# Performance work log

Hardware: AMD Instinct MI355X
Metric: run time of the kernel (lower is better)

The kernel has to match this reference:

```python
import jax, jax.numpy as jnp
import numpy as np

IMG = 128
NEAR, FAR = 1.0, 100.0
BG_EPS = 1e-3      # eps in soft_rasterize: background depth logit
SIGMA = 1e-6       # sigma_val
DIST_EPS = 1e-4    # dist_eps
GAMMA = 1e-6       # gamma_val
CHUNK = 500
B, V, F = 1, 5023, 10000


def setup_inputs():
    key = jax.random.key(0)
    k1, k2, k3, k4 = jax.random.split(key, 4)
    xy = jax.random.uniform(k1, (B, V, 2), minval=-1.0, maxval=1.0, dtype=jnp.float32)
    z = jax.random.uniform(k2, (B, V, 1), minval=5.0, maxval=15.0, dtype=jnp.float32)
    vertices = jnp.concatenate([xy, z], axis=-1)              # [B,V,3]
    faces = jax.random.randint(k3, (B, F, 3), 0, V, dtype=jnp.int32)
    attributes = jax.random.uniform(k4, (B, F, 3, 3), dtype=jnp.float32)
    return {"vertices": vertices, "faces": faces, "attributes": attributes}


def _seg_dist2(px, py, ax, ay, bx, by):
    # squared distance from pixel (px,py) to segment a-b; broadcasts [P] vs [B,C,1]
    dx = px - ax; dy = py - ay
    ex = bx - ax; ey = by - ay
    l2 = jnp.maximum(ex * ex + ey * ey, 1e-12)
    t = jnp.clip((dx * ex + dy * ey) / l2, 0.0, 1.0)
    rx = dx - t * ex; ry = dy - t * ey
    return rx * rx + ry * ry


def _render(vertices, faces, attributes):
    is_ = IMG
    P = is_ * is_
    bz = vertices.shape[0]
    v = vertices.at[..., 0].multiply(-1.0)                    # x flip (in-place in torch)
    fv = jax.vmap(lambda vv, ff: vv[ff])(v, faces)            # [B,F,3vert,3xyz]
    tex = attributes[..., :3]                                 # [B,F,3vert,3rgb]
    # fill_back=True: append copies with reversed winding
    fv = jnp.concatenate([fv, fv[:, :, ::-1, :]], axis=1)     # [B,2F,3,3]
    tex = jnp.concatenate([tex, tex[:, :, ::-1, :]], axis=1)
    F2 = fv.shape[1]
    pad = (-F2) % CHUNK
    valid = jnp.concatenate([jnp.ones((F2,), bool), jnp.zeros((pad,), bool)])
    fv = jnp.pad(fv, ((0, 0), (0, pad), (0, 0), (0, 0)))
    tex = jnp.pad(tex, ((0, 0), (0, pad), (0, 0), (0, 0)))
    n_chunks = (F2 + pad) // CHUNK
    fv = jnp.transpose(fv.reshape(bz, n_chunks, CHUNK, 3, 3), (1, 0, 2, 3, 4))
    tex = jnp.transpose(tex.reshape(bz, n_chunks, CHUNK, 3, 3), (1, 0, 2, 3, 4))
    valid = valid.reshape(n_chunks, CHUNK)

    # pixel centers in [-1,1]; row 0 is the top of the image (y flipped as in CUDA)
    xs = (2.0 * jnp.arange(is_, dtype=jnp.float32) + 1.0 - is_) / is_
    ys = (2.0 * (is_ - 1 - jnp.arange(is_, dtype=jnp.float32)) + 1.0 - is_) / is_
    px = jnp.broadcast_to(xs[None, :], (is_, is_)).reshape(-1)  # [P]
    py = jnp.broadcast_to(ys[:, None], (is_, is_)).reshape(-1)

    thr = DIST_EPS * SIGMA
    inv_g = 1.0 / GAMMA

    def step(carry, inp):
        m, s, cacc, prod = carry                # [B,P],[B,P],[B,3,P],[B,P]
        fvc, txc, vld = inp                     # [B,C,3,3],[B,C,3,3],[C]
        x0 = fvc[:, :, 0, 0][..., None]; y0 = fvc[:, :, 0, 1][..., None]; z0 = fvc[:, :, 0, 2][..., None]
        x1 = fvc[:, :, 1, 0][..., None]; y1 = fvc[:, :, 1, 1][..., None]; z1 = fvc[:, :, 1, 2][..., None]
        x2 = fvc[:, :, 2, 0][..., None]; y2 = fvc[:, :, 2, 1][..., None]; z2 = fvc[:, :, 2, 2][..., None]
        det = (y1 - y2) * (x0 - x2) + (x2 - x1) * (y0 - y2)   # [B,C,1]
        det = jnp.where(jnp.abs(det) < 1e-10, jnp.where(det < 0, -1e-10, 1e-10), det)
        w0 = ((y1 - y2) * (px - x2) + (x2 - x1) * (py - y2)) / det  # [B,C,P]
        w1 = ((y2 - y0) * (px - x2) + (x0 - x2) * (py - y2)) / det
        w2 = 1.0 - w0 - w1
        inside = (w0 >= 0) & (w1 >= 0) & (w2 >= 0)
        dis = jnp.minimum(jnp.minimum(_seg_dist2(px, py, x0, y0, x1, y1),
                                      _seg_dist2(px, py, x1, y1, x2, y2)),
                          _seg_dist2(px, py, x2, y2, x0, y0))     # [B,C,P] squared dist
        contrib = (inside | (dis < thr)) & vld[None, :, None]
        sgn = jnp.where(inside, 1.0, -1.0)
        Dp = jnp.where(contrib, jax.nn.sigmoid(sgn * dis / SIGMA), 0.0)
        prod = prod * jnp.prod(1.0 - Dp, axis=1)                  # alpha: prod(1-D)
        # clipped barycentric + perspective-correct depth
        c0 = jnp.clip(w0, 0.0, 1.0); c1 = jnp.clip(w1, 0.0, 1.0); c2 = jnp.clip(w2, 0.0, 1.0)
        csum = jnp.maximum(c0 + c1 + c2, 1e-5)
        c0 = c0 / csum; c1 = c1 / csum; c2 = c2 / csum
        zp_inv = c0 / z0 + c1 / z1 + c2 / z2
        zp = 1.0 / jnp.where(jnp.abs(zp_inv) < 1e-12, 1e-12, zp_inv)
        front = (y2 - y0) * (x1 - x0) < (y1 - y0) * (x2 - x0)     # [B,C,1]
        rgb_m = contrib & front & (zp >= NEAR) & (zp <= FAR)
        zpn = (FAR - zp) / (FAR - NEAR)
        new_m = jnp.maximum(m, jnp.max(jnp.where(rgb_m, zpn, -jnp.inf), axis=1))
        e = jnp.exp(jnp.where(rgb_m, (zpn - new_m[:, None, :]) * inv_g, -jnp.inf)) * Dp
        scale = jnp.exp((m - new_m) * inv_g)                      # [B,P]
        wc = jnp.stack([c0, c1, c2], axis=2)                      # [B,C,3,P]
        col = jnp.einsum('bcvp,bcvk->bckp', wc, txc)              # interpolated rgb
        s = s * scale + jnp.sum(e, axis=1)
        cacc = cacc * scale[:, None, :] + jnp.sum(e[:, :, None, :] * col, axis=1)
        return (new_m, s, cacc, prod), None

    m0 = jnp.full((bz, P), BG_EPS, jnp.float32)   # background logit = eps
    s0 = jnp.ones((bz, P), jnp.float32)           # exp((eps - m0)/gamma) = 1
    c0_ = jnp.zeros((bz, 3, P), jnp.float32)      # black background
    p0 = jnp.ones((bz, P), jnp.float32)
    (m, s, cacc, prod), _ = jax.lax.scan(jax.checkpoint(step), (m0, s0, c0_, p0), (fv, tex, valid))
    rgb = cacc / s[:, None, :]
    alpha = 1.0 - prod
    return jnp.concatenate([rgb, alpha[:, None, :]], axis=1).reshape(bz, 4, is_, is_)


def reference(vertices, faces, attributes):
    return _render(vertices, faces, attributes)
```

## Files before the change

kernel.cpp:

```cpp
#include <hip/hip_runtime.h>
#include <math.h>


#define NFACE 10000
#define IMG   128
#define P_TOT (IMG*IMG)
#define FSTR  40
#define NTILE 64
#define NQ    4
#define CAPQ  2500
#define CAP   (CAPQ*NQ)
#define BMAX  4096
#define NB    1024
#define CH    256
#define NCH   40
#define Z_LO  0.85f
#define Z_W   (0.12f/1024.0f)

__device__ __forceinline__ float rcp_nr(float x) {
    float r = __builtin_amdgcn_rcpf(x);
    r = r * __builtin_fmaf(-x, r, 2.0f);
    return r;
}

__device__ __forceinline__ float segd(float px, float py, float ax, float ay,
                                      float bx, float by, float il) {
    float dx = px - ax, dy = py - ay;
    float ex = bx - ax, ey = by - ay;
    float t = (dx * ex + dy * ey) * il;
    t = fminf(fmaxf(t, 0.0f), 1.0f);
    float rx = dx - t * ex, ry = dy - t * ey;
    return rx * rx + ry * ry;
}

__device__ __forceinline__ float rfl_f(float x) {
    return __uint_as_float(__builtin_amdgcn_readfirstlane(__float_as_uint(x)));
}

__device__ __forceinline__ int zbucket(float zub) {
    int b = (int)((zub - Z_LO) * (1.0f / Z_W));
    return min(max(b, 0), NB - 1);
}

__global__ __launch_bounds__(256) void k_prehist(const float* __restrict__ v,
                                                 const int* __restrict__ fc,
                                                 const float* __restrict__ at,
                                                 float* __restrict__ fb,
                                                 int* __restrict__ hist) {
    __shared__ int lh[NB];
    int c = blockIdx.x, tid = threadIdx.x;
    for (int j = tid; j < NB; j += 256) lh[j] = 0;
    __syncthreads();

    int f = c * CH + tid;
    if (f < NFACE) {
        int i0 = fc[3 * f], i1 = fc[3 * f + 1], i2 = fc[3 * f + 2];
        float x0 = -v[3 * i0], y0 = v[3 * i0 + 1], z0 = v[3 * i0 + 2];
        float x1 = -v[3 * i1], y1 = v[3 * i1 + 1], z1 = v[3 * i1 + 2];
        float x2 = -v[3 * i2], y2 = v[3 * i2 + 1], z2 = v[3 * i2 + 2];

        float det = (y1 - y2) * (x0 - x2) + (x2 - x1) * (y0 - y2);
        if (fabsf(det) < 1e-10f) det = (det < 0.0f) ? -1e-10f : 1e-10f;
        float a0 = y1 - y2, b0 = x2 - x1, a1 = y2 - y0, b1 = x0 - x2, detp = det;
        if (det < 0.0f) { detp = -det; a0 = -a0; b0 = -b0; a1 = -a1; b1 = -b1; }

        float a2 = a0 + a1, b2 = b0 + b1;
        float g0 = fmaxf(sqrtf(a0 * a0 + b0 * b0), 1e-12f);
        float g1 = fmaxf(sqrtf(a1 * a1 + b1 * b1), 1e-12f);
        float g2 = fmaxf(sqrtf(a2 * a2 + b2 * b2), 1e-12f);
        const float MARG = 3e-5f, AG = 1e-9f;
        float m0 = -(MARG * g0 + AG), m1 = -(MARG * g1 + AG), m2 = -(MARG * g2 + AG);

        float e01x = x1 - x0, e01y = y1 - y0;
        float e12x = x2 - x1, e12y = y2 - y1;
        float e20x = x0 - x2, e20y = y0 - y2;
        float il01 = 1.0f / fmaxf(e01x * e01x + e01y * e01y, 1e-12f);
        float il12 = 1.0f / fmaxf(e12x * e12x + e12y * e12y, 1e-12f);
        float il20 = 1.0f / fmaxf(e20x * e20x + e20y * e20y, 1e-12f);

        const float BM = 2e-5f;
        float bxmin = fminf(fminf(x0, x1), x2) - BM, bxmax = fmaxf(fmaxf(x0, x1), x2) + BM;
        float bymin = fminf(fminf(y0, y1), y2) - BM, bymax = fmaxf(fmaxf(y0, y1), y2) + BM;

        int mult = (((y2 - y0) * (x1 - x0)) < ((y1 - y0) * (x2 - x0)))
                 + (((y0 - y2) * (x1 - x2)) < ((y1 - y2) * (x0 - x2)));

        float zmin = fminf(fminf(z0, z1), z2);
        float zub = (100.0f - zmin) / 99.0f + 2e-6f;

        float* F = fb + (size_t)f * FSTR;
        F[0] = bxmin; F[1] = bxmax; F[2] = bymin; F[3] = bymax;
        F[4] = x2; F[5] = y2; F[6] = a0; F[7] = b0;
        F[8] = a1; F[9] = b1; F[10] = detp; F[11] = zub;
        F[12] = m0; F[13] = m1; F[14] = m2; F[15] = (float)mult;
        F[16] = x0; F[17] = y0; F[18] = x1; F[19] = y1;
        F[20] = il01; F[21] = il12; F[22] = il20; F[23] = 1.0f / detp;
        F[24] = 1.0f / z0; F[25] = 1.0f / z1; F[26] = 1.0f / z2;
        F[27] = 1.0f / g0; F[28] = 1.0f / g1; F[29] = 1.0f / g2;
#pragma unroll
        for (int k = 0; k < 9; k++) F[30 + k] = at[(size_t)f * 9 + k];
        F[39] = 0.0f;

        atomicAdd(&lh[zbucket(zub)], 1);
    }
    __syncthreads();
    for (int j = tid; j < NB; j += 256) hist[c * NB + j] = lh[j];
}

__global__ __launch_bounds__(1024) void k_scan(int* __restrict__ hist) {
    __shared__ int a[NB];
    int t = threadIdx.x;
    int tot = 0;
    for (int c = 0; c < NCH; c++) tot += hist[c * NB + t];
    a[t] = tot;
    for (int off = 1; off < NB; off <<= 1) {
        __syncthreads();
        int v = a[t] + ((t + off < NB) ? a[t + off] : 0);
        __syncthreads();
        a[t] = v;
    }
    int r = a[t] - tot;
    for (int c = 0; c < NCH; c++) {
        int h = hist[c * NB + t];
        hist[c * NB + t] = r;
        r += h;
    }
}

__global__ __launch_bounds__(256) void k_scatterre(const float* __restrict__ fb,
                                                   const int* __restrict__ hist,
                                                   float* __restrict__ fb2) {
    __shared__ int sb[CH];
    int c = blockIdx.x, tid = threadIdx.x;
    int f = c * CH + tid;
    bool valid = (f < NFACE);
    int b = valid ? zbucket(fb[(size_t)f * FSTR + 11]) : -1;
    sb[tid] = b;
    __syncthreads();
    if (valid) {
        int rank = 0;
        for (int j = 0; j < CH; j++) {
            int v2 = sb[j];
            rank += (j < tid && v2 == b) ? 1 : 0;
        }
        int pos = hist[c * NB + b] + rank;
        const float4* src = (const float4*)(fb + (size_t)f * FSTR);
        float4* dst = (float4*)(fb2 + (size_t)pos * FSTR);
#pragma unroll
        for (int k = 0; k < 10; k++) dst[k] = src[k];
        fb2[(size_t)pos * FSTR + 11] = Z_LO + (float)(b + 1) * Z_W + 1e-7f;
    }
}

__global__ __launch_bounds__(256) void k_bin(const float* __restrict__ fb2,
                                             float2* __restrict__ tmeta,
                                             int* __restrict__ cnt4) {
    int t = blockIdx.x >> 2, q = blockIdx.x & 3;
    int tid = threadIdx.x, wv = tid >> 6, lane = tid & 63;
    int tx = t & 7, ty = t >> 3;
    float x_lo = (float)(2 * (tx * 16) + 1 - IMG) / (float)IMG;
    float x_hi = (float)(2 * (tx * 16 + 15) + 1 - IMG) / (float)IMG;
    float y_hi = (float)(127 - 2 * (ty * 16)) / (float)IMG;
    float y_lo = (float)(127 - 2 * (ty * 16 + 15)) / (float)IMG;
    float cx = 0.5f * (x_lo + x_hi), hx = 0.5f * (x_hi - x_lo);
    float cy = 0.5f * (y_lo + y_hi), hy = 0.5f * (y_hi - y_lo);

    __shared__ int wc[4];
    int cnt = 0;
    int f0 = q * CAPQ;
    for (int base = f0; base < f0 + CAPQ; base += 256) {
        int j = base + tid;
        bool ov = false;
        float zub = 0.0f;
        if (j < f0 + CAPQ) {
            const float4* H = (const float4*)(fb2 + (size_t)j * FSTR);
            float4 h0 = H[0], h1 = H[1], h2 = H[2], h3 = H[3];
            ov = (h0.x <= x_hi) & (h0.y >= x_lo) & (h0.z <= y_hi) & (h0.w >= y_lo);
            if (ov) {
                float dx = cx - h1.x, dy = cy - h1.y;
                float mx0 = h1.z * dx + h1.w * dy + fabsf(h1.z) * hx + fabsf(h1.w) * hy;
                float mx1 = h2.x * dx + h2.y * dy + fabsf(h2.x) * hx + fabsf(h2.y) * hy;
                float A2 = -(h1.z + h2.x), B2 = -(h1.w + h2.y);
                float mx2 = h2.z + A2 * dx + B2 * dy + fabsf(A2) * hx + fabsf(B2) * hy;
                ov = (mx0 >= h3.x) & (mx1 >= h3.y) & (mx2 >= h3.z);
                zub = h2.w;
            }
        }
        unsigned long long mask = __ballot(ov);
        if (lane == 0) wc[wv] = __popcll(mask);
        __syncthreads();
        int off = cnt;
        for (int w = 0; w < 4; ++w) {
            if (w < wv) off += wc[w];
        }
        if (ov) {
            int pos = off + __popcll(mask & ((1ull << lane) - 1ull));
            tmeta[(size_t)t * CAP + q * CAPQ + pos] =
                make_float2(zub, __int_as_float(j));
        }
        cnt += wc[0] + wc[1] + wc[2] + wc[3];
        __syncthreads();
    }
    if (tid == 0) cnt4[t * 4 + q] = cnt;
}

__device__ __forceinline__ void derive_map(const int* __restrict__ cnt4,
                                           int B, int tid, int nthr,
                                           int* sLen, int* sS, int* sP,
                                           int* sUsed) {
    if (tid < NTILE)
        sLen[tid] = cnt4[4 * tid] + cnt4[4 * tid + 1]
                  + cnt4[4 * tid + 2] + cnt4[4 * tid + 3];
    __syncthreads();
    if (tid == 0) {
        int tot = 0;
        for (int k = 0; k < NTILE; k++) tot += sLen[k];
        tot = max(tot, 1);
        int acc = 0;
        for (int k = 0; k < NTILE; k++) {
            int S = max(1, (int)(((long long)sLen[k] * (long long)(B - NTILE)) /
                                 (long long)tot));
            sS[k] = S; sP[k] = acc; acc += S;
        }
        *sUsed = acc;
    }
    __syncthreads();
}

__global__ __launch_bounds__(256) void k_main(const float* __restrict__ fb2,
                                              const float2* __restrict__ tmeta,
                                              const int* __restrict__ cnt4,
                                              float* __restrict__ part,
                                              int B) {
    __shared__ int sLen[NTILE], sS[NTILE], sP[NTILE], sUsed;
    int tid = threadIdx.x;
    derive_map(cnt4, B, tid, 256, sLen, sS, sP, &sUsed);
    int bid = blockIdx.x;
    if (bid >= sUsed) return;
    int lo = 0, hi = NTILE - 1;
    while (lo < hi) {
        int mid = (lo + hi + 1) >> 1;
        if (sP[mid] <= bid) lo = mid; else hi = mid - 1;
    }
    int t = lo, seg = bid - sP[lo];
    int S = sS[t];

    int wv = tid >> 6, lane = tid & 63;
    int tx = t & 7, ty = t >> 3;
    int col = tx * 16 + (wv & 1) * 8 + (lane & 7);
    int row = ty * 16 + (wv >> 1) * 8 + (lane >> 3);
    float px = (float)(2 * col + 1 - IMG) / (float)IMG;
    float py = (float)(2 * (IMG - 1 - row) + 1 - IMG) / (float)IMG;

    const float2* pm = tmeta + (size_t)t * CAP;

    float m = -__builtin_inff();
    float s = 0.0f, ca = 0.0f, cb = 0.0f, cc = 0.0f, pr = 1.0f;

    const float NEAR_T = 4.3e-3f;
    const float ZM = 1.3e-4f;

    auto EVAL = [&](int fj, float zcur, float4 g0, float4 g1, float4 g2, float4 g3) {
        bool inbox = (px >= g0.x) & (px <= g0.y) & (py >= g0.z) & (py <= g0.w);
        if (!__any(inbox)) return;

        float x2 = g1.x, y2 = g1.y;
        float dx2 = px - x2, dy2 = py - y2;
        float num0 = g1.z * dx2 + g1.w * dy2;
        float num1 = g2.x * dx2 + g2.y * dy2;
        float detp = g2.z;
        float num2 = detp - num0 - num1;
        bool maybe = inbox & (num0 >= g3.x) & (num1 >= g3.y) & (num2 >= g3.z);
        if (!__any(maybe)) return;

        const float* F = fb2 + (size_t)fj * FSTR;

        bool inside = (num0 >= 0.0f) & (num1 >= 0.0f) & (num2 >= 0.0f);
        bool inside_l = inside & inbox;

        float lin0 = num0 * F[27];
        float lin1 = num1 * F[28];
        float lin2 = num2 * F[29];
        float lbmin = fminf(fminf(lin0, lin1), lin2);

        bool outNear = maybe & (!inside);
        bool nearIn  = inside_l & (lbmin < NEAR_T);
        bool anyNear = __any(nearIn | outNear);

        float dis = 1e9f;
        float Dp;
        if (anyNear) {
            bool needAll = __any(outNear);
            float x0 = F[16], y0 = F[17], x1 = F[18], y1 = F[19];
            float d01 = 1e9f, d12 = 1e9f, d20 = 1e9f;
            if (needAll | __any(inside_l & (lin2 < NEAR_T)))
                d01 = segd(px, py, x0, y0, x1, y1, F[20]);
            if (needAll | __any(inside_l & (lin0 < NEAR_T)))
                d12 = segd(px, py, x1, y1, x2, y2, F[21]);
            if (needAll | __any(inside_l & (lin1 < NEAR_T)))
                d20 = segd(px, py, x2, y2, x0, y0, F[22]);
            dis = fminf(fminf(d01, d12), d20);

            float qq = dis * 1e6f;
            float xs_ = inside ? qq : -qq;
            float tt = __expf(-fabsf(xs_));
            float Dpn = (xs_ >= 0.0f ? 1.0f : tt) * rcp_nr(1.0f + tt);
            bool nearl = nearIn | outNear;
            Dp = nearl ? Dpn : (inside_l ? 1.0f : 0.0f);
        } else {
            Dp = inside_l ? 1.0f : 0.0f;
        }

        bool contrib = inside_l | (outNear & (dis < 1e-10f));
        Dp = contrib ? Dp : 0.0f;
        float omd = 1.0f - Dp;
        pr *= contrib ? (omd * omd) : 1.0f;

        float multf = g3.w;
        bool doz = contrib & (multf > 0.0f);
        if (__any(doz & (zcur > m - ZM))) {
            float rdetp = F[23];
            float w0 = num0 * rdetp;
            float w1 = num1 * rdetp;
            float c0 = fminf(fmaxf(w0, 0.0f), 1.0f);
            float c1 = fminf(fmaxf(w1, 0.0f), 1.0f);
            float c2 = fminf(fmaxf(1.0f - w0 - w1, 0.0f), 1.0f);
            float csum = fmaxf(c0 + c1 + c2, 1e-5f);
            float rcs = rcp_nr(csum);
            c0 *= rcs; c1 *= rcs; c2 *= rcs;
            float zpi = c0 * F[24] + c1 * F[25] + c2 * F[26];
            if (fabsf(zpi) < 1e-12f) zpi = 1e-12f;
            float zp = rcp_nr(zpi);
            if (doz & (zp >= 1.0f) & (zp <= 100.0f)) {
                float zpn = (100.0f - zp) / 99.0f;
                if (zpn > m) {
                    float scl = __expf((m - zpn) * 1e6f);
                    s *= scl; ca *= scl; cb *= scl; cc *= scl;
                    m = zpn;
                }
                float arg = (zpn - m) * 1e6f;
                if (arg > -110.0f) {
                    float e = __expf(arg) * Dp * multf;
                    float col0 = c0 * F[30] + c1 * F[33] + c2 * F[36];
                    float col1 = c0 * F[31] + c1 * F[34] + c2 * F[37];
                    float col2 = c0 * F[32] + c1 * F[35] + c2 * F[38];
                    s += e; ca += e * col0; cb += e * col1; cc += e * col2;
                }
            }
        }
    };

    bool done = false;
    for (int q = 0; q < 4 && !done; ++q) {
        int qlen = cnt4[t * 4 + q];
        const float2* pq = pm + q * CAPQ;
        int i = seg;
        while (i < qlen) {
            float2 mt0 = pq[i];
            int i1 = i + S;
            bool has1 = (i1 < qlen);
            float2 mt1 = has1 ? pq[i1] : mt0;
            float z0 = rfl_f(mt0.x);
            int   f0 = __builtin_amdgcn_readfirstlane(__float_as_int(mt0.y));
            float z1 = rfl_f(mt1.x);
            int   f1 = __builtin_amdgcn_readfirstlane(__float_as_int(mt1.y));
            const float4* H0 = (const float4*)(fb2 + (size_t)f0 * FSTR);
            const float4* H1 = (const float4*)(fb2 + (size_t)f1 * FSTR);
            float4 a0 = H0[0], a1 = H0[1], a2 = H0[2], a3 = H0[3];
            float4 b0 = H1[0], b1 = H1[1], b2 = H1[2], b3 = H1[3];

            if (__all((pr == 0.0f) & (z0 <= m - ZM))) { done = true; break; }
            EVAL(f0, z0, a0, a1, a2, a3);
            if (has1) {
                if (__all((pr == 0.0f) & (z1 <= m - ZM))) { done = true; break; }
                EVAL(f1, z1, b0, b1, b2, b3);
            }
            i += 2 * S;
        }
    }

    size_t pb = ((size_t)(bid * 4 + wv) * 6) * 64;
    part[pb + 0 * 64 + lane] = m;
    part[pb + 1 * 64 + lane] = s;
    part[pb + 2 * 64 + lane] = ca;
    part[pb + 3 * 64 + lane] = cb;
    part[pb + 4 * 64 + lane] = cc;
    part[pb + 5 * 64 + lane] = pr;
}

__global__ __launch_bounds__(1024) void k_reduce(const float* __restrict__ part,
                                                 const int* __restrict__ cnt4,
                                                 float* __restrict__ out,
                                                 int B) {
    __shared__ int sLen[NTILE], sS[NTILE], sP[NTILE], sUsed;
    __shared__ float sm[4][256], ss[4][256], sa[4][256], sb2[4][256],
                     sc[4][256], sp[4][256];
    int t = blockIdx.x;
    int tid = threadIdx.x;
    derive_map(cnt4, B, tid, 1024, sLen, sS, sP, &sUsed);
    int start = sP[t], S = sS[t];

    int pid = tid & 255, sub = tid >> 8;
    int qd = pid >> 6, lane = pid & 63;

    const float NINF = -__builtin_inff();
    float mp = NINF;
    for (int sgi = sub; sgi < S; sgi += 4)
        mp = fmaxf(mp, part[(((size_t)(start + sgi) * 4 + qd) * 6 + 0) * 64 + lane]);
    float sum = 0.0f, a = 0.0f, b = 0.0f, c = 0.0f, pr = 1.0f;
    for (int sgi = sub; sgi < S; sgi += 4) {
        const float* rp = part + (((size_t)(start + sgi) * 4 + qd) * 6) * 64;
        float rm = rp[0 * 64 + lane];
        float w = (rm == NINF) ? 0.0f : __expf((rm - mp) * 1e6f);
        pr *= rp[5 * 64 + lane];
        if (__any(w != 0.0f)) {
            sum += rp[1 * 64 + lane] * w;
            a += rp[2 * 64 + lane] * w;
            b += rp[3 * 64 + lane] * w;
            c += rp[4 * 64 + lane] * w;
        }
    }
    sm[sub][pid] = mp; ss[sub][pid] = sum; sa[sub][pid] = a;
    sb2[sub][pid] = b; sc[sub][pid] = c;  sp[sub][pid] = pr;
    __syncthreads();
    if (sub == 0) {
        int tx = t & 7, ty = t >> 3;
        int col = tx * 16 + (qd & 1) * 8 + (lane & 7);
        int row = ty * 16 + (qd >> 1) * 8 + (lane >> 3);
        int p = row * IMG + col;
        float M = 0.001f;
#pragma unroll
        for (int k = 0; k < 4; k++) M = fmaxf(M, sm[k][pid]);
        float SUM = __expf((0.001f - M) * 1e6f);
        float A = 0.0f, B2 = 0.0f, C = 0.0f, PR = 1.0f;
#pragma unroll
        for (int k = 0; k < 4; k++) {
            float w = __expf((sm[k][pid] - M) * 1e6f);
            SUM += ss[k][pid] * w;
            A += sa[k][pid] * w;
            B2 += sb2[k][pid] * w;
            C += sc[k][pid] * w;
            PR *= sp[k][pid];
        }
        out[0 * P_TOT + p] = A / SUM;
        out[1 * P_TOT + p] = B2 / SUM;
        out[2 * P_TOT + p] = C / SUM;
        out[3 * P_TOT + p] = 1.0f - PR;
    }
}

extern "C" void kernel_launch(void* const* d_in, const int* in_sizes, int n_in,
                              void* d_out, int out_size, void* d_ws, size_t ws_size,
                              hipStream_t stream) {
    const float* verts = (const float*)d_in[0];
    const int*   faces = (const int*)d_in[1];
    const float* attrs = (const float*)d_in[2];
    float* out = (float*)d_out;
    float* ws  = (float*)d_ws;

    float*  fb    = ws;
    int*    hist  = (int*)(fb + (size_t)NFACE * FSTR);
    float*  fb2   = (float*)(hist + NCH * NB);
    float2* tmeta = (float2*)(fb2 + (size_t)NFACE * FSTR);
    int*    cnt4  = (int*)(tmeta + (size_t)NTILE * CAP);
    float*  part  = (float*)(cnt4 + NTILE * 4);

    size_t used_f = 2 * (size_t)NFACE * FSTR + NCH * NB
                  + 2 * (size_t)NTILE * CAP + NTILE * 4;
    long   rem_f  = (long)(ws_size / 4) - (long)used_f;
    int B = (int)(rem_f / (6 * 256));
    if (B > BMAX) B = BMAX;
    if (B < 256)  B = 256;

    k_prehist<<<NCH, 256, 0, stream>>>(verts, faces, attrs, fb, hist);
    k_scan<<<1, 1024, 0, stream>>>(hist);
    k_scatterre<<<NCH, 256, 0, stream>>>(fb, hist, fb2);
    k_bin<<<NTILE * NQ, 256, 0, stream>>>(fb2, tmeta, cnt4);
    k_main<<<B, 256, 0, stream>>>(fb2, tmeta, cnt4, part, B);
    k_reduce<<<NTILE, 1024, 0, stream>>>(part, cnt4, out, B);
}
```

Measured before the change: 148.9 us.

## Bin faces per 8x8 sub-quadrant and skip non-overlapping faces per wave

The binning kernel now tests each face against the four 8x8 quadrants of a 16x16 tile and packs a 4-bit quadrant mask into the high bits of the stored face index. In the main kernel each wave covers one quadrant, checks its bit, and skips faces that do not touch its quadrant before loading the face header. The two-face software-pipelined loop is replaced by a simple one-face loop, which gives up the prefetch of the next face's header in exchange for cheaper culling. It also drops the j<f0+CAPQ bounds guard in binning, which is safe only if the buffer sizes line up.

```diff
diff --git a/kernel.cpp b/kernel.cpp
--- a/kernel.cpp
+++ b/kernel.cpp
@@ -162,8 +162,20 @@
     float x_hi = (float)(2 * (tx * 16 + 15) + 1 - IMG) / (float)IMG;
     float y_hi = (float)(127 - 2 * (ty * 16)) / (float)IMG;
     float y_lo = (float)(127 - 2 * (ty * 16 + 15)) / (float)IMG;
-    float cx = 0.5f * (x_lo + x_hi), hx = 0.5f * (x_hi - x_lo);
-    float cy = 0.5f * (y_lo + y_hi), hy = 0.5f * (y_hi - y_lo);
+
+    float qxlo[4], qxhi[4], qylo[4], qyhi[4], qcx[4], qcy[4], qhx[4], qhy[4];
+#pragma unroll
+    for (int rl = 0; rl < 4; rl++) {
+        int qx = rl & 1, qy = rl >> 1;
+        int c0 = tx * 16 + qx * 8, r0 = ty * 16 + qy * 8;
+        float xl = (float)(2 * c0 + 1 - IMG) / (float)IMG;
+        float xh = (float)(2 * (c0 + 7) + 1 - IMG) / (float)IMG;
+        float yh = (float)(127 - 2 * r0) / (float)IMG;
+        float yl = (float)(127 - 2 * (r0 + 7)) / (float)IMG;
+        qxlo[rl] = xl; qxhi[rl] = xh; qylo[rl] = yl; qyhi[rl] = yh;
+        qcx[rl] = 0.5f * (xl + xh); qhx[rl] = 0.5f * (xh - xl);
+        qcy[rl] = 0.5f * (yl + yh); qhy[rl] = 0.5f * (yh - yl);
+    }
 
     __shared__ int wc[4];
     int cnt = 0;
@@ -171,18 +183,29 @@
     for (int base = f0; base < f0 + CAPQ; base += 256) {
         int j = base + tid;
         bool ov = false;
+        int qmask = 0;
         float zub = 0.0f;
-        if (j < f0 + CAPQ) {
+        {
             const float4* H = (const float4*)(fb2 + (size_t)j * FSTR);
             float4 h0 = H[0], h1 = H[1], h2 = H[2], h3 = H[3];
-            ov = (h0.x <= x_hi) & (h0.y >= x_lo) & (h0.z <= y_hi) & (h0.w >= y_lo);
-            if (ov) {
-                float dx = cx - h1.x, dy = cy - h1.y;
-                float mx0 = h1.z * dx + h1.w * dy + fabsf(h1.z) * hx + fabsf(h1.w) * hy;
-                float mx1 = h2.x * dx + h2.y * dy + fabsf(h2.x) * hx + fabsf(h2.y) * hy;
+            bool tov = (h0.x <= x_hi) & (h0.y >= x_lo) & (h0.z <= y_hi) & (h0.w >= y_lo);
+            if (tov) {
                 float A2 = -(h1.z + h2.x), B2 = -(h1.w + h2.y);
-                float mx2 = h2.z + A2 * dx + B2 * dy + fabsf(A2) * hx + fabsf(B2) * hy;
-                ov = (mx0 >= h3.x) & (mx1 >= h3.y) & (mx2 >= h3.z);
+#pragma unroll
+                for (int rl = 0; rl < 4; rl++) {
+                    bool o = (h0.x <= qxhi[rl]) & (h0.y >= qxlo[rl]) &
+                             (h0.z <= qyhi[rl]) & (h0.w >= qylo[rl]);
+                    if (o) {
+                        float dx = qcx[rl] - h1.x, dy = qcy[rl] - h1.y;
+                        float hx = qhx[rl], hy = qhy[rl];
+                        float mx0 = h1.z * dx + h1.w * dy + fabsf(h1.z) * hx + fabsf(h1.w) * hy;
+                        float mx1 = h2.x * dx + h2.y * dy + fabsf(h2.x) * hx + fabsf(h2.y) * hy;
+                        float mx2 = h2.z + A2 * dx + B2 * dy + fabsf(A2) * hx + fabsf(B2) * hy;
+                        o = (mx0 >= h3.x) & (mx1 >= h3.y) & (mx2 >= h3.z);
+                    }
+                    qmask |= (o ? 1 : 0) << rl;
+                }
+                ov = (qmask != 0);
                 zub = h2.w;
             }
         }
@@ -196,7 +219,7 @@
         if (ov) {
             int pos = off + __popcll(mask & ((1ull << lane) - 1ull));
             tmeta[(size_t)t * CAP + q * CAPQ + pos] =
-                make_float2(zub, __int_as_float(j));
+                make_float2(zub, __int_as_float(j | (qmask << 20)));
         }
         cnt += wc[0] + wc[1] + wc[2] + wc[3];
         __syncthreads();
@@ -205,7 +228,7 @@
 }
 
 __device__ __forceinline__ void derive_map(const int* __restrict__ cnt4,
-                                           int B, int tid, int nthr,
+                                           int B, int tid,
                                            int* sLen, int* sS, int* sP,
                                            int* sUsed) {
     if (tid < NTILE)
@@ -234,7 +257,7 @@
                                               int B) {
     __shared__ int sLen[NTILE], sS[NTILE], sP[NTILE], sUsed;
     int tid = threadIdx.x;
-    derive_map(cnt4, B, tid, 256, sLen, sS, sP, &sUsed);
+    derive_map(cnt4, B, tid, sLen, sS, sP, &sUsed);
     int bid = blockIdx.x;
     if (bid >= sUsed) return;
     int lo = 0, hi = NTILE - 1;
@@ -259,123 +282,110 @@
 
     const float NEAR_T = 4.3e-3f;
     const float ZM = 1.3e-4f;
-
-    auto EVAL = [&](int fj, float zcur, float4 g0, float4 g1, float4 g2, float4 g3) {
-        bool inbox = (px >= g0.x) & (px <= g0.y) & (py >= g0.z) & (py <= g0.w);
-        if (!__any(inbox)) return;
-
-        float x2 = g1.x, y2 = g1.y;
-        float dx2 = px - x2, dy2 = py - y2;
-        float num0 = g1.z * dx2 + g1.w * dy2;
-        float num1 = g2.x * dx2 + g2.y * dy2;
-        float detp = g2.z;
-        float num2 = detp - num0 - num1;
-        bool maybe = inbox & (num0 >= g3.x) & (num1 >= g3.y) & (num2 >= g3.z);
-        if (!__any(maybe)) return;
-
-        const float* F = fb2 + (size_t)fj * FSTR;
-
-        bool inside = (num0 >= 0.0f) & (num1 >= 0.0f) & (num2 >= 0.0f);
-        bool inside_l = inside & inbox;
-
-        float lin0 = num0 * F[27];
-        float lin1 = num1 * F[28];
-        float lin2 = num2 * F[29];
-        float lbmin = fminf(fminf(lin0, lin1), lin2);
-
-        bool outNear = maybe & (!inside);
-        bool nearIn  = inside_l & (lbmin < NEAR_T);
-        bool anyNear = __any(nearIn | outNear);
-
-        float dis = 1e9f;
-        float Dp;
-        if (anyNear) {
-            bool needAll = __any(outNear);
-            float x0 = F[16], y0 = F[17], x1 = F[18], y1 = F[19];
-            float d01 = 1e9f, d12 = 1e9f, d20 = 1e9f;
-            if (needAll | __any(inside_l & (lin2 < NEAR_T)))
-                d01 = segd(px, py, x0, y0, x1, y1, F[20]);
-            if (needAll | __any(inside_l & (lin0 < NEAR_T)))
-                d12 = segd(px, py, x1, y1, x2, y2, F[21]);
-            if (needAll | __any(inside_l & (lin1 < NEAR_T)))
-                d20 = segd(px, py, x2, y2, x0, y0, F[22]);
-            dis = fminf(fminf(d01, d12), d20);
-
-            float qq = dis * 1e6f;
-            float xs_ = inside ? qq : -qq;
-            float tt = __expf(-fabsf(xs_));
-            float Dpn = (xs_ >= 0.0f ? 1.0f : tt) * rcp_nr(1.0f + tt);
-            bool nearl = nearIn | outNear;
-            Dp = nearl ? Dpn : (inside_l ? 1.0f : 0.0f);
-        } else {
-            Dp = inside_l ? 1.0f : 0.0f;
-        }
-
-        bool contrib = inside_l | (outNear & (dis < 1e-10f));
-        Dp = contrib ? Dp : 0.0f;
-        float omd = 1.0f - Dp;
-        pr *= contrib ? (omd * omd) : 1.0f;
-
-        float multf = g3.w;
-        bool doz = contrib & (multf > 0.0f);
-        if (__any(doz & (zcur > m - ZM))) {
-            float rdetp = F[23];
-            float w0 = num0 * rdetp;
-            float w1 = num1 * rdetp;
-            float c0 = fminf(fmaxf(w0, 0.0f), 1.0f);
-            float c1 = fminf(fmaxf(w1, 0.0f), 1.0f);
-            float c2 = fminf(fmaxf(1.0f - w0 - w1, 0.0f), 1.0f);
-            float csum = fmaxf(c0 + c1 + c2, 1e-5f);
-            float rcs = rcp_nr(csum);
-            c0 *= rcs; c1 *= rcs; c2 *= rcs;
-            float zpi = c0 * F[24] + c1 * F[25] + c2 * F[26];
-            if (fabsf(zpi) < 1e-12f) zpi = 1e-12f;
-            float zp = rcp_nr(zpi);
-            if (doz & (zp >= 1.0f) & (zp <= 100.0f)) {
-                float zpn = (100.0f - zp) / 99.0f;
-                if (zpn > m) {
-                    float scl = __expf((m - zpn) * 1e6f);
-                    s *= scl; ca *= scl; cb *= scl; cc *= scl;
-                    m = zpn;
-                }
-                float arg = (zpn - m) * 1e6f;
-                if (arg > -110.0f) {
-                    float e = __expf(arg) * Dp * multf;
-                    float col0 = c0 * F[30] + c1 * F[33] + c2 * F[36];
-                    float col1 = c0 * F[31] + c1 * F[34] + c2 * F[37];
-                    float col2 = c0 * F[32] + c1 * F[35] + c2 * F[38];
-                    s += e; ca += e * col0; cb += e * col1; cc += e * col2;
-                }
-            }
-        }
-    };
+    const int mybit = 1 << (20 + wv);
 
     bool done = false;
     for (int q = 0; q < 4 && !done; ++q) {
         int qlen = cnt4[t * 4 + q];
         const float2* pq = pm + q * CAPQ;
-        int i = seg;
-        while (i < qlen) {
-            float2 mt0 = pq[i];
-            int i1 = i + S;
-            bool has1 = (i1 < qlen);
-            float2 mt1 = has1 ? pq[i1] : mt0;
-            float z0 = rfl_f(mt0.x);
-            int   f0 = __builtin_amdgcn_readfirstlane(__float_as_int(mt0.y));
-            float z1 = rfl_f(mt1.x);
-            int   f1 = __builtin_amdgcn_readfirstlane(__float_as_int(mt1.y));
-            const float4* H0 = (const float4*)(fb2 + (size_t)f0 * FSTR);
-            const float4* H1 = (const float4*)(fb2 + (size_t)f1 * FSTR);
-            float4 a0 = H0[0], a1 = H0[1], a2 = H0[2], a3 = H0[3];
-            float4 b0 = H1[0], b1 = H1[1], b2 = H1[2], b3 = H1[3];
-
-            if (__all((pr == 0.0f) & (z0 <= m - ZM))) { done = true; break; }
-            EVAL(f0, z0, a0, a1, a2, a3);
-            if (has1) {
-                if (__all((pr == 0.0f) & (z1 <= m - ZM))) { done = true; break; }
-                EVAL(f1, z1, b0, b1, b2, b3);
+        for (int i = seg; i < qlen; i += S) {
+            float2 mt = pq[i];
+            float zcur = rfl_f(mt.x);
+            if (__all((pr == 0.0f) & (zcur <= m - ZM))) { done = true; break; }
+            int raw = __builtin_amdgcn_readfirstlane(__float_as_int(mt.y));
+            if (!(raw & mybit)) continue;
+            int fj = raw & 0xFFFFF;
+
+            const float4* H = (const float4*)(fb2 + (size_t)fj * FSTR);
+            float4 g0 = H[0], g1 = H[1], g2 = H[2], g3 = H[3];
+
+            bool inbox = (px >= g0.x) & (px <= g0.y) & (py >= g0.z) & (py <= g0.w);
+            if (!__any(inbox)) continue;
+
+            float x2 = g1.x, y2 = g1.y;
+            float dx2 = px - x2, dy2 = py - y2;
+            float num0 = g1.z * dx2 + g1.w * dy2;
+            float num1 = g2.x * dx2 + g2.y * dy2;
+            float detp = g2.z;
+            float num2 = detp - num0 - num1;
+            bool maybe = inbox & (num0 >= g3.x) & (num1 >= g3.y) & (num2 >= g3.z);
+            if (!__any(maybe)) continue;
+
+            const float* F = fb2 + (size_t)fj * FSTR;
+
+            bool inside = (num0 >= 0.0f) & (num1 >= 0.0f) & (num2 >= 0.0f);
+            bool inside_l = inside & inbox;
+
+            float lin0 = num0 * F[27];
+            float lin1 = num1 * F[28];
+            float lin2 = num2 * F[29];
+            float lbmin = fminf(fminf(lin0, lin1), lin2);
+
+            bool outNear = maybe & (!inside);
+            bool nearIn  = inside_l & (lbmin < NEAR_T);
+            bool anyNear = __any(nearIn | outNear);
+
+            float dis = 1e9f;
+            float Dp;
+            if (anyNear) {
+                bool needAll = __any(outNear);
+                float x0 = F[16], y0 = F[17], x1 = F[18], y1 = F[19];
+                float d01 = 1e9f, d12 = 1e9f, d20 = 1e9f;
+                if (needAll | __any(inside_l & (lin2 < NEAR_T)))
+                    d01 = segd(px, py, x0, y0, x1, y1, F[20]);
+                if (needAll | __any(inside_l & (lin0 < NEAR_T)))
+                    d12 = segd(px, py, x1, y1, x2, y2, F[21]);
+                if (needAll | __any(inside_l & (lin1 < NEAR_T)))
+                    d20 = segd(px, py, x2, y2, x0, y0, F[22]);
+                dis = fminf(fminf(d01, d12), d20);
+
+                float qq = dis * 1e6f;
+                float xs_ = inside ? qq : -qq;
+                float tt = __expf(-fabsf(xs_));
+                float Dpn = (xs_ >= 0.0f ? 1.0f : tt) * rcp_nr(1.0f + tt);
+                bool nearl = nearIn | outNear;
+                Dp = nearl ? Dpn : (inside_l ? 1.0f : 0.0f);
+            } else {
+                Dp = inside_l ? 1.0f : 0.0f;
             }
-            i += 2 * S;
+
+            bool contrib = inside_l | (outNear & (dis < 1e-10f));
+            Dp = contrib ? Dp : 0.0f;
+            float omd = 1.0f - Dp;
+            pr *= contrib ? (omd * omd) : 1.0f;
+
+            float multf = g3.w;
+            bool doz = contrib & (multf > 0.0f);
+            if (__any(doz & (zcur > m - ZM))) {
+                float rdetp = F[23];
+                float w0 = num0 * rdetp;
+                float w1 = num1 * rdetp;
+                float c0 = fminf(fmaxf(w0, 0.0f), 1.0f);
+                float c1 = fminf(fmaxf(w1, 0.0f), 1.0f);
+                float c2 = fminf(fmaxf(1.0f - w0 - w1, 0.0f), 1.0f);
+                float csum = fmaxf(c0 + c1 + c2, 1e-5f);
+                float rcs = rcp_nr(csum);
+                c0 *= rcs; c1 *= rcs; c2 *= rcs;
+                float zpi = c0 * F[24] + c1 * F[25] + c2 * F[26];
+                if (fabsf(zpi) < 1e-12f) zpi = 1e-12f;
+                float zp = rcp_nr(zpi);
+                if (doz & (zp >= 1.0f) & (zp <= 100.0f)) {
+                    float zpn = (100.0f - zp) / 99.0f;
+                    if (zpn > m) {
+                        float scl = __expf((m - zpn) * 1e6f);
+                        s *= scl; ca *= scl; cb *= scl; cc *= scl;
+                        m = zpn;
+                    }
+                    float arg = (zpn - m) * 1e6f;
+                    if (arg > -110.0f) {
+                        float e = __expf(arg) * Dp * multf;
+                        float col0 = c0 * F[30] + c1 * F[33] + c2 * F[36];
+                        float col1 = c0 * F[31] + c1 * F[34] + c2 * F[37];
+                        float col2 = c0 * F[32] + c1 * F[35] + c2 * F[38];
+                        s += e; ca += e * col0; cb += e * col1; cc += e * col2;
+                    }
+                }
+            }
         }
     }
 
@@ -397,7 +407,7 @@
                      sc[4][256], sp[4][256];
     int t = blockIdx.x;
     int tid = threadIdx.x;
-    derive_map(cnt4, B, tid, 1024, sLen, sS, sP, &sUsed);
+    derive_map(cnt4, B, tid, sLen, sS, sP, &sUsed);
     int start = sP[t], S = sS[t];
 
     int pid = tid & 255, sub = tid >> 8;
```

Measured after the change: 158.5 us. +6.4%, slower.
